# Kernel optimization log

Measured on AMD Instinct MI355X. Metric: run time of the kernel, lower is better.

The kernel has to match this reference:

```python
import jax, jax.numpy as jnp
import numpy as np

B, T, D, H, HD, I = 256, 1, 2048, 16, 128, 5504
EPS = 1e-6
ROPE_THETA = 10000.0


def setup_inputs() -> dict:
    key = jax.random.key(0)
    ks = jax.random.split(key, 20)
    W = 0.02  # weight init scale
    hidden_states = jax.random.normal(ks[0], (B, T, D), jnp.float32)
    # RoPE tables for each batch element at a distinct decode position
    pos = jnp.arange(B, dtype=jnp.float32) % 4096.0
    inv_freq = 1.0 / (ROPE_THETA ** (jnp.arange(0, HD, 2, dtype=jnp.float32) / HD))
    ang = pos[:, None] * inv_freq[None, :]                      # [B, HD/2]
    emb = jnp.concatenate([ang, ang], axis=-1)                  # [B, HD]
    cos = jnp.cos(emb)[:, None, :]                              # [B, 1, HD]
    sin = jnp.sin(emb)[:, None, :]
    n = lambda k, s: jax.random.normal(k, s, jnp.float32) * W
    return {
        'hidden_states': hidden_states, 'cos': cos, 'sin': sin,
        'router_w': n(ks[1], (D,)), 'router_b': jnp.zeros((1,), jnp.float32),
        'ln1_w': jnp.ones((D,), jnp.float32), 'ln2_w': jnp.ones((D,), jnp.float32),
        'wq': n(ks[2], (D, D)), 'bq': jnp.zeros((D,), jnp.float32),
        'wk': n(ks[3], (D, D)), 'bk': jnp.zeros((D,), jnp.float32),
        'wv': n(ks[4], (D, D)), 'bv': jnp.zeros((D,), jnp.float32),
        'wo': n(ks[5], (D, D)),
        'w_gate': n(ks[6], (D, I)), 'w_up': n(ks[7], (D, I)), 'w_down': n(ks[8], (I, D)),
        'k_sel': 128,
    }


def _rms(x, w):
    v = jnp.mean(jnp.square(x), axis=-1, keepdims=True)
    return x * jax.lax.rsqrt(v + EPS) * w


def _rotate_half(x):
    x1, x2 = jnp.split(x, 2, axis=-1)
    return jnp.concatenate([-x2, x1], axis=-1)


def _decoder_layer(x, cs, sn, ln1_w, ln2_w, wq, bq, wk, bk, wv, bv, wo, w_gate, w_up, w_down):
    # x: [k, T, D]; cs/sn: [k, T, HD]
    k = x.shape[0]
    h = _rms(x, ln1_w)
    q = (h @ wq + bq).reshape(k, T, H, HD).transpose(0, 2, 1, 3)  # [k,H,T,HD]
    kk = (h @ wk + bk).reshape(k, T, H, HD).transpose(0, 2, 1, 3)
    v = (h @ wv + bv).reshape(k, T, H, HD).transpose(0, 2, 1, 3)
    c = cs[:, None, :, :]  # [k,1,T,HD]
    s = sn[:, None, :, :]
    q = q * c + _rotate_half(q) * s
    kk = kk * c + _rotate_half(kk) * s
    att = jnp.einsum('bhqd,bhkd->bhqk', q, kk) * (HD ** -0.5)
    p = jax.nn.softmax(att, axis=-1)  # T==1: trivial causal mask
    o = jnp.einsum('bhqk,bhkd->bhqd', p, v).transpose(0, 2, 1, 3).reshape(k, T, D) @ wo
    x = x + o
    h2 = _rms(x, ln2_w)
    mlp = (jax.nn.silu(h2 @ w_gate) * (h2 @ w_up)) @ w_down
    return x + mlp


def reference(hidden_states, cos, sin, router_w, router_b, ln1_w, ln2_w,
              wq, bq, wk, bk, wv, bv, wo, w_gate, w_up, w_down, k_sel):
    # causal router: linear D->1 scores per batch row (T==1 decode step)
    scores = hidden_states[:, 0, :] @ router_w + router_b[0]   # [B]
    probs = jax.nn.sigmoid(scores)
    _, sel_idx = jax.lax.top_k(probs, k_sel)                   # [k]
    x_sel = hidden_states[sel_idx]                             # gather [k,T,D]
    cs, sn = cos[sel_idx], sin[sel_idx]                        # [k,T,HD]
    x_out = _decoder_layer(x_sel, cs, sn, ln1_w, ln2_w, wq, bq, wk, bk,
                           wv, bv, wo, w_gate, w_up, w_down)
    return hidden_states.at[sel_idx].set(x_out)                # scatter back
```

## Files before the change

### kernel.cpp

```cpp
#include <hip/hip_runtime.h>
#include <hip/hip_bf16.h>
#include <stdint.h>


#define D_ 2048
#define I_ 5504
#define NROWS 256
#define KSEL 128

typedef __attribute__((ext_vector_type(8))) short short8;
typedef __attribute__((ext_vector_type(4))) float floatx4;

__device__ __forceinline__ unsigned short f2bf(float f) {
  union { float f; unsigned int u; } v; v.f = f;
  unsigned int r = (v.u + 0x7FFFu + ((v.u >> 16) & 1u)) >> 16;
  return (unsigned short)r;
}

__device__ __forceinline__ unsigned int pk2(float lo, float hi) {
  __hip_bfloat162 h = __float22bfloat162_rn(float2{lo, hi});
  unsigned int u; __builtin_memcpy(&u, &h, 4); return u;
}

__global__ void k_router(const float* __restrict__ hid, const float* __restrict__ rw,
                         const float* __restrict__ rb, float* __restrict__ scores) {
  int b = blockIdx.x, t = threadIdx.x;
  const float* x = hid + (size_t)b * D_;
  float s = 0.f;
  for (int i = t; i < D_; i += 256) s += x[i] * rw[i];
  for (int o = 32; o; o >>= 1) s += __shfl_down(s, o);
  __shared__ float red[4];
  if ((t & 63) == 0) red[t >> 6] = s;
  __syncthreads();
  if (t == 0) scores[b] = red[0] + red[1] + red[2] + red[3] + rb[0];
}

__global__ void k_select(const float* __restrict__ scores, const int* __restrict__ kptr,
                         int* __restrict__ sel, int* __restrict__ pos) {
  __shared__ float sv[NROWS];
  int t = threadIdx.x;
  sv[t] = scores[t];
  __syncthreads();
  float s = sv[t];
  int c = 0;
  for (int j = 0; j < NROWS; ++j) {
    float o = sv[j];
    c += (o > s) || (o == s && j < t);
  }
  int k = *kptr;
  if (c < k) sel[c] = t;
  pos[t] = (c < k) ? c : -1;
}

__global__ void k_rms1(const float* __restrict__ hid, const int* __restrict__ sel,
                       const float* __restrict__ ln1, const float* __restrict__ bv,
                       unsigned short* __restrict__ Hb, float* __restrict__ V,
                       float* __restrict__ X1) {
  int i = blockIdx.x, t = threadIdx.x;
  int r = sel[i];
  const float* x = hid + (size_t)r * D_;
  float xs[8]; float ss = 0.f;
#pragma unroll
  for (int c = 0; c < 8; ++c) { float v = x[t + c * 256]; xs[c] = v; ss += v * v; }
  for (int o = 32; o; o >>= 1) ss += __shfl_down(ss, o);
  __shared__ float red[4];
  if ((t & 63) == 0) red[t >> 6] = ss;
  __syncthreads();
  float inv = rsqrtf((red[0] + red[1] + red[2] + red[3]) * (1.0f / D_) + 1e-6f);
#pragma unroll
  for (int c = 0; c < 8; ++c) {
    int idx = t + c * 256;
    size_t o_ = (size_t)i * D_ + idx;
    Hb[o_] = f2bf(xs[c] * inv * ln1[idx]);
    V[o_] = bv[idx];
    X1[o_] = xs[c];
  }
}

__global__ void k_rms2(const float* __restrict__ X1, const float* __restrict__ ln2,
                       unsigned short* __restrict__ H2b, float* __restrict__ G,
                       float* __restrict__ U) {
  int i = blockIdx.x, t = threadIdx.x;
  const float* x = X1 + (size_t)i * D_;
  float xs[8]; float ss = 0.f;
#pragma unroll
  for (int c = 0; c < 8; ++c) { float v = x[t + c * 256]; xs[c] = v; ss += v * v; }
  for (int o = 32; o; o >>= 1) ss += __shfl_down(ss, o);
  __shared__ float red[4];
  if ((t & 63) == 0) red[t >> 6] = ss;
  __syncthreads();
  float inv = rsqrtf((red[0] + red[1] + red[2] + red[3]) * (1.0f / D_) + 1e-6f);
#pragma unroll
  for (int c = 0; c < 8; ++c) {
    int idx = t + c * 256;
    H2b[(size_t)i * D_ + idx] = f2bf(xs[c] * inv * ln2[idx]);
  }
  for (int j = t; j < I_; j += 256) {
    G[(size_t)i * I_ + j] = 0.f;
    U[(size_t)i * I_ + j] = 0.f;
  }
}

__global__ void k_silu_out(const float* __restrict__ G, const float* __restrict__ U,
                           unsigned short* __restrict__ Mb,
                           const float* __restrict__ X1, const int* __restrict__ pos,
                           const float* __restrict__ hid, float* __restrict__ out) {
  int tid = blockIdx.x * 256 + threadIdx.x;
  int stride = gridDim.x * 256;
  const int nM = KSEL * I_;
  for (int i = tid; i < nM; i += stride) {
    float g = G[i], u = U[i];
    float m = (g / (1.f + expf(-g))) * u;
    Mb[i] = f2bf(m);
  }
  const int nO4 = NROWS * (D_ / 4);
  const float4* X14 = (const float4*)X1;
  const float4* H4 = (const float4*)hid;
  float4* O4 = (float4*)out;
  for (int i = tid; i < nO4; i += stride) {
    int row = i >> 9;
    int c4 = i & 511;
    int p = pos[row];
    O4[i] = (p >= 0) ? X14[(size_t)p * 512 + c4] : H4[i];
  }
}

template<bool AF32, bool DUAL>
__global__ __launch_bounds__(256, 2)
void k_gemm(const void* __restrict__ Ap, const float* __restrict__ B0,
            const float* __restrict__ B1, float* __restrict__ C0,
            float* __restrict__ C1, const int* __restrict__ rowmap,
            int K, int KA, int Kb, int lda, int N, int KT, int ldc) {
  constexpr int ST = 72;
  const int bn = blockIdx.x;
  const int kt0 = blockIdx.y * KT;
  const int kt1 = kt0 + KT;
  const int tid = threadIdx.x;
  const int lane = tid & 63;
  const int wave = tid >> 6;
  const int wm = wave >> 1, wn = wave & 1;
  const int fm = lane & 15, kq = lane >> 4;

  __shared__ alignas(16) unsigned short Asm[128 * ST];
  __shared__ alignas(16) unsigned short Bsm0[32 * ST];
  __shared__ alignas(16) unsigned short Bsm1[DUAL ? 32 * ST : 8];

  floatx4 acc0[4] = {};
  floatx4 acc1[4] = {};

  const int ar = tid >> 1;
  const int ah = (tid & 1) * 32;
  const int bnn = tid & 31;
  const int bk8 = (tid >> 5) * 8;

  const unsigned short* Ab = AF32 ? nullptr : (const unsigned short*)Ap + (size_t)ar * lda + ah;
  const float*          Af = AF32 ? (const float*)Ap + (size_t)ar * lda + ah : nullptr;
  const float* B0c = B0 + (size_t)(bn * 32 + bnn);
  const float* B1c = DUAL ? B1 + (size_t)(bn * 32 + bnn) : nullptr;

  uint4 a4[4];
  float4 af8[8];
  float b0v[8], b1v[8];

  auto load_tile = [&](int kt) {
    if (AF32) {
#pragma unroll
      for (int r = 0; r < 8; ++r) {
        int c0 = kt + ah + r * 4;
        af8[r] = (c0 < KA) ? *(const float4*)(Af + kt + r * 4)
                           : make_float4(0.f, 0.f, 0.f, 0.f);
      }
    } else {
#pragma unroll
      for (int r = 0; r < 4; ++r) {
        int c0 = kt + ah + r * 8;
        a4[r] = (c0 < KA) ? *(const uint4*)(Ab + kt + r * 8)
                          : make_uint4(0u, 0u, 0u, 0u);
      }
    }
#pragma unroll
    for (int j = 0; j < 8; ++j) {
      int kr = kt + bk8 + j; kr = kr < Kb ? kr : Kb - 1;
      b0v[j] = B0c[(size_t)kr * N];
      if (DUAL) b1v[j] = B1c[(size_t)kr * N];
    }
  };

  load_tile(kt0);

  for (int kt = kt0; kt < kt1; kt += 64) {
    __syncthreads();
    {
      uint4* Ad = (uint4*)&Asm[ar * ST + ah];
      if (AF32) {
        uint4 q;
#pragma unroll
        for (int r = 0; r < 4; ++r) {
          q.x = pk2(af8[2 * r].x, af8[2 * r].y);
          q.y = pk2(af8[2 * r].z, af8[2 * r].w);
          q.z = pk2(af8[2 * r + 1].x, af8[2 * r + 1].y);
          q.w = pk2(af8[2 * r + 1].z, af8[2 * r + 1].w);
          Ad[r] = q;
        }
      } else {
#pragma unroll
        for (int r = 0; r < 4; ++r) Ad[r] = a4[r];
      }
      uint4 bq;
      bq.x = pk2(b0v[0], b0v[1]); bq.y = pk2(b0v[2], b0v[3]);
      bq.z = pk2(b0v[4], b0v[5]); bq.w = pk2(b0v[6], b0v[7]);
      *(uint4*)&Bsm0[bnn * ST + bk8] = bq;
      if (DUAL) {
        uint4 cq;
        cq.x = pk2(b1v[0], b1v[1]); cq.y = pk2(b1v[2], b1v[3]);
        cq.z = pk2(b1v[4], b1v[5]); cq.w = pk2(b1v[6], b1v[7]);
        *(uint4*)&Bsm1[bnn * ST + bk8] = cq;
      }
    }
    __syncthreads();
    if (kt + 64 < kt1) load_tile(kt + 64);
    short8 afr[2][4], bf0[2], bf1[2];
#pragma unroll
    for (int s = 0; s < 2; ++s) {
#pragma unroll
      for (int i = 0; i < 4; ++i)
        afr[s][i] = *(const short8*)&Asm[(wm * 64 + i * 16 + fm) * ST + s * 32 + kq * 8];
      bf0[s] = *(const short8*)&Bsm0[(wn * 16 + fm) * ST + s * 32 + kq * 8];
      if (DUAL)
        bf1[s] = *(const short8*)&Bsm1[(wn * 16 + fm) * ST + s * 32 + kq * 8];
    }
#pragma unroll
    for (int s = 0; s < 2; ++s) {
#pragma unroll
      for (int i = 0; i < 4; ++i) {
        acc0[i] = __builtin_amdgcn_mfma_f32_16x16x32_bf16(afr[s][i], bf0[s], acc0[i], 0, 0, 0);
        if (DUAL)
          acc1[i] = __builtin_amdgcn_mfma_f32_16x16x32_bf16(afr[s][i], bf1[s], acc1[i], 0, 0, 0);
      }
    }
  }

#pragma unroll
  for (int i = 0; i < 4; ++i) {
#pragma unroll
    for (int r = 0; r < 4; ++r) {
      int row = wm * 64 + i * 16 + kq * 4 + r;
      size_t rbase = rowmap ? (size_t)rowmap[row] * ldc : (size_t)row * ldc;
      int col = bn * 32 + wn * 16 + fm;
      atomicAdd(&C0[rbase + col], acc0[i][r]);
      if (DUAL) atomicAdd(&C1[rbase + col], acc1[i][r]);
    }
  }
}

extern "C" void kernel_launch(void* const* d_in, const int* in_sizes, int n_in,
                              void* d_out, int out_size, void* d_ws, size_t ws_size,
                              hipStream_t stream) {
  const float* hid = (const float*)d_in[0];
  const float* rw  = (const float*)d_in[3];
  const float* rb  = (const float*)d_in[4];
  const float* ln1 = (const float*)d_in[5];
  const float* ln2 = (const float*)d_in[6];
  const float* wv  = (const float*)d_in[11];
  const float* bv  = (const float*)d_in[12];
  const float* wo  = (const float*)d_in[13];
  const float* wg  = (const float*)d_in[14];
  const float* wu  = (const float*)d_in[15];
  const float* wd  = (const float*)d_in[16];
  const int*   kp  = (const int*)d_in[17];
  float* out = (float*)d_out;

  char* ws = (char*)d_ws;
  float*          scores = (float*)(ws + 0);
  int*            sel    = (int*)(ws + 1024);
  int*            pos    = (int*)(ws + 1536);
  unsigned short* Hb     = (unsigned short*)(ws + 4096);
  float*          V      = (float*)(ws + 528384);
  float*          X1     = (float*)(ws + 1576960);
  unsigned short* H2b    = (unsigned short*)(ws + 2625536);
  float*          G      = (float*)(ws + 3149824);
  float*          U      = (float*)(ws + 5967872);
  unsigned short* Mb     = (unsigned short*)(ws + 8785920);

  k_router<<<256, 256, 0, stream>>>(hid, rw, rb, scores);
  k_select<<<1, 256, 0, stream>>>(scores, kp, sel, pos);
  k_rms1<<<128, 256, 0, stream>>>(hid, sel, ln1, bv, Hb, V, X1);
  k_gemm<false, false><<<dim3(64, 8), 256, 0, stream>>>(
      Hb, wv, nullptr, V, nullptr, nullptr, 2048, 2048, 2048, 2048, 2048, 256, 2048);
  k_gemm<true, false><<<dim3(64, 8), 256, 0, stream>>>(
      V, wo, nullptr, X1, nullptr, nullptr, 2048, 2048, 2048, 2048, 2048, 256, 2048);
  k_rms2<<<128, 256, 0, stream>>>(X1, ln2, H2b, G, U);
  k_gemm<false, true><<<dim3(172, 4), 256, 0, stream>>>(
      H2b, wg, wu, G, U, nullptr, 2048, 2048, 2048, 2048, 5504, 512, 5504);
  k_silu_out<<<1024, 256, 0, stream>>>(G, U, Mb, X1, pos, hid, out);
  k_gemm<false, false><<<dim3(64, 8), 256, 0, stream>>>(
      Mb, wd, nullptr, out, nullptr, sel, 5632, 5504, 5504, 5504, 2048, 704, 2048);
}
```

Before: 294.8 us.

## Replace LDS-tiled split-K GEMM with register double-buffered direct-load MFMA kernel

The GEMM no longer stages tiles in shared memory. Each wave now loads its A fragments and the fp32 B columns straight into registers, double-buffers them across 32-wide K steps, and feeds MFMA on 16-column output tiles. Block IDs are remapped in an XCD-aware way, and shapes become template constants. The change also zeroes G/U in one separate vectorized kernel, vectorizes the router, RMSNorm and SiLU kernels with float4/packed-bf16 stores, and drops the padded K in the down projection. It removes LDS round-trips and barriers, at the cost of redundant B loads across the waves of a block and more atomics per output column.

```diff
diff --git a/kernel.cpp b/kernel.cpp
--- a/kernel.cpp
+++ b/kernel.cpp
@@ -11,23 +11,28 @@
 typedef __attribute__((ext_vector_type(8))) short short8;
 typedef __attribute__((ext_vector_type(4))) float floatx4;
 
-__device__ __forceinline__ unsigned short f2bf(float f) {
-  union { float f; unsigned int u; } v; v.f = f;
-  unsigned int r = (v.u + 0x7FFFu + ((v.u >> 16) & 1u)) >> 16;
-  return (unsigned short)r;
-}
-
 __device__ __forceinline__ unsigned int pk2(float lo, float hi) {
   __hip_bfloat162 h = __float22bfloat162_rn(float2{lo, hi});
   unsigned int u; __builtin_memcpy(&u, &h, 4); return u;
 }
 
+__global__ void k_zero(float4* __restrict__ p, int n4) {
+  int i = blockIdx.x * 256 + threadIdx.x;
+  int st = gridDim.x * 256;
+  for (; i < n4; i += st) p[i] = float4{0.f, 0.f, 0.f, 0.f};
+}
+
 __global__ void k_router(const float* __restrict__ hid, const float* __restrict__ rw,
                          const float* __restrict__ rb, float* __restrict__ scores) {
   int b = blockIdx.x, t = threadIdx.x;
-  const float* x = hid + (size_t)b * D_;
+  const float4* x4 = (const float4*)(hid + (size_t)b * D_);
+  const float4* w4 = (const float4*)rw;
   float s = 0.f;
-  for (int i = t; i < D_; i += 256) s += x[i] * rw[i];
+#pragma unroll
+  for (int c = 0; c < 2; ++c) {
+    float4 xv = x4[t + c * 256], wv = w4[t + c * 256];
+    s += xv.x * wv.x + xv.y * wv.y + xv.z * wv.z + xv.w * wv.w;
+  }
   for (int o = 32; o; o >>= 1) s += __shfl_down(s, o);
   __shared__ float red[4];
   if ((t & 63) == 0) red[t >> 6] = s;
@@ -58,47 +63,50 @@
                        float* __restrict__ X1) {
   int i = blockIdx.x, t = threadIdx.x;
   int r = sel[i];
-  const float* x = hid + (size_t)r * D_;
-  float xs[8]; float ss = 0.f;
-#pragma unroll
-  for (int c = 0; c < 8; ++c) { float v = x[t + c * 256]; xs[c] = v; ss += v * v; }
+  const float4* x4 = (const float4*)(hid + (size_t)r * D_);
+  float4 xa = x4[2 * t], xb = x4[2 * t + 1];
+  float ss = xa.x * xa.x + xa.y * xa.y + xa.z * xa.z + xa.w * xa.w
+           + xb.x * xb.x + xb.y * xb.y + xb.z * xb.z + xb.w * xb.w;
   for (int o = 32; o; o >>= 1) ss += __shfl_down(ss, o);
   __shared__ float red[4];
   if ((t & 63) == 0) red[t >> 6] = ss;
   __syncthreads();
   float inv = rsqrtf((red[0] + red[1] + red[2] + red[3]) * (1.0f / D_) + 1e-6f);
-#pragma unroll
-  for (int c = 0; c < 8; ++c) {
-    int idx = t + c * 256;
-    size_t o_ = (size_t)i * D_ + idx;
-    Hb[o_] = f2bf(xs[c] * inv * ln1[idx]);
-    V[o_] = bv[idx];
-    X1[o_] = xs[c];
-  }
+  const float4* w4 = (const float4*)ln1;
+  float4 wa = w4[2 * t], wb = w4[2 * t + 1];
+  union { unsigned int u[4]; uint4 q; } pk;
+  pk.u[0] = pk2(xa.x * inv * wa.x, xa.y * inv * wa.y);
+  pk.u[1] = pk2(xa.z * inv * wa.z, xa.w * inv * wa.w);
+  pk.u[2] = pk2(xb.x * inv * wb.x, xb.y * inv * wb.y);
+  pk.u[3] = pk2(xb.z * inv * wb.z, xb.w * inv * wb.w);
+  ((uint4*)(Hb + (size_t)i * D_))[t] = pk.q;
+  const float4* b4 = (const float4*)bv;
+  float4* V4 = (float4*)(V + (size_t)i * D_);
+  V4[2 * t] = b4[2 * t]; V4[2 * t + 1] = b4[2 * t + 1];
+  float4* X4 = (float4*)(X1 + (size_t)i * D_);
+  X4[2 * t] = xa; X4[2 * t + 1] = xb;
 }
 
 __global__ void k_rms2(const float* __restrict__ X1, const float* __restrict__ ln2,
-                       unsigned short* __restrict__ H2b, float* __restrict__ G,
-                       float* __restrict__ U) {
+                       unsigned short* __restrict__ H2b) {
   int i = blockIdx.x, t = threadIdx.x;
-  const float* x = X1 + (size_t)i * D_;
-  float xs[8]; float ss = 0.f;
-#pragma unroll
-  for (int c = 0; c < 8; ++c) { float v = x[t + c * 256]; xs[c] = v; ss += v * v; }
+  const float4* x4 = (const float4*)(X1 + (size_t)i * D_);
+  float4 xa = x4[2 * t], xb = x4[2 * t + 1];
+  float ss = xa.x * xa.x + xa.y * xa.y + xa.z * xa.z + xa.w * xa.w
+           + xb.x * xb.x + xb.y * xb.y + xb.z * xb.z + xb.w * xb.w;
   for (int o = 32; o; o >>= 1) ss += __shfl_down(ss, o);
   __shared__ float red[4];
   if ((t & 63) == 0) red[t >> 6] = ss;
   __syncthreads();
   float inv = rsqrtf((red[0] + red[1] + red[2] + red[3]) * (1.0f / D_) + 1e-6f);
-#pragma unroll
-  for (int c = 0; c < 8; ++c) {
-    int idx = t + c * 256;
-    H2b[(size_t)i * D_ + idx] = f2bf(xs[c] * inv * ln2[idx]);
-  }
-  for (int j = t; j < I_; j += 256) {
-    G[(size_t)i * I_ + j] = 0.f;
-    U[(size_t)i * I_ + j] = 0.f;
-  }
+  const float4* w4 = (const float4*)ln2;
+  float4 wa = w4[2 * t], wb = w4[2 * t + 1];
+  union { unsigned int u[4]; uint4 q; } pk;
+  pk.u[0] = pk2(xa.x * inv * wa.x, xa.y * inv * wa.y);
+  pk.u[1] = pk2(xa.z * inv * wa.z, xa.w * inv * wa.w);
+  pk.u[2] = pk2(xb.x * inv * wb.x, xb.y * inv * wb.y);
+  pk.u[3] = pk2(xb.z * inv * wb.z, xb.w * inv * wb.w);
+  ((uint4*)(H2b + (size_t)i * D_))[t] = pk.q;
 }
 
 __global__ void k_silu_out(const float* __restrict__ G, const float* __restrict__ U,
@@ -106,149 +114,142 @@
                            const float* __restrict__ X1, const int* __restrict__ pos,
                            const float* __restrict__ hid, float* __restrict__ out) {
   int tid = blockIdx.x * 256 + threadIdx.x;
-  int stride = gridDim.x * 256;
-  const int nM = KSEL * I_;
-  for (int i = tid; i < nM; i += stride) {
-    float g = G[i], u = U[i];
-    float m = (g / (1.f + expf(-g))) * u;
-    Mb[i] = f2bf(m);
+  const int nM4 = KSEL * I_ / 4;
+  if (tid < nM4) {
+    float4 g = ((const float4*)G)[tid], u = ((const float4*)U)[tid];
+    float m0 = (g.x / (1.f + expf(-g.x))) * u.x;
+    float m1 = (g.y / (1.f + expf(-g.y))) * u.y;
+    float m2 = (g.z / (1.f + expf(-g.z))) * u.z;
+    float m3 = (g.w / (1.f + expf(-g.w))) * u.w;
+    uint2 o; o.x = pk2(m0, m1); o.y = pk2(m2, m3);
+    ((uint2*)Mb)[tid] = o;
   }
   const int nO4 = NROWS * (D_ / 4);
-  const float4* X14 = (const float4*)X1;
-  const float4* H4 = (const float4*)hid;
-  float4* O4 = (float4*)out;
-  for (int i = tid; i < nO4; i += stride) {
-    int row = i >> 9;
-    int c4 = i & 511;
+  if (tid < nO4) {
+    int row = tid >> 9;
+    int c4 = tid & 511;
     int p = pos[row];
-    O4[i] = (p >= 0) ? X14[(size_t)p * 512 + c4] : H4[i];
-  }
-}
-
-template<bool AF32, bool DUAL>
-__global__ __launch_bounds__(256, 2)
+    ((float4*)out)[tid] = (p >= 0) ? ((const float4*)X1)[(size_t)p * 512 + c4]
+                                   : ((const float4*)hid)[tid];
+  }
+}
+
+template<bool AF32, bool DUAL, int SPLITS, int LDA, int NN, int LDC>
+__global__ __launch_bounds__(256, 3)
 void k_gemm(const void* __restrict__ Ap, const float* __restrict__ B0,
             const float* __restrict__ B1, float* __restrict__ C0,
             float* __restrict__ C1, const int* __restrict__ rowmap,
-            int K, int KA, int Kb, int lda, int N, int KT, int ldc) {
-  constexpr int ST = 72;
-  const int bn = blockIdx.x;
-  const int kt0 = blockIdx.y * KT;
-  const int kt1 = kt0 + KT;
-  const int tid = threadIdx.x;
-  const int lane = tid & 63;
-  const int wave = tid >> 6;
-  const int wm = wave >> 1, wn = wave & 1;
-  const int fm = lane & 15, kq = lane >> 4;
-
-  __shared__ alignas(16) unsigned short Asm[128 * ST];
-  __shared__ alignas(16) unsigned short Bsm0[32 * ST];
-  __shared__ alignas(16) unsigned short Bsm1[DUAL ? 32 * ST : 8];
-
-  floatx4 acc0[4] = {};
-  floatx4 acc1[4] = {};
-
-  const int ar = tid >> 1;
-  const int ah = (tid & 1) * 32;
-  const int bnn = tid & 31;
-  const int bk8 = (tid >> 5) * 8;
-
-  const unsigned short* Ab = AF32 ? nullptr : (const unsigned short*)Ap + (size_t)ar * lda + ah;
-  const float*          Af = AF32 ? (const float*)Ap + (size_t)ar * lda + ah : nullptr;
-  const float* B0c = B0 + (size_t)(bn * 32 + bnn);
-  const float* B1c = DUAL ? B1 + (size_t)(bn * 32 + bnn) : nullptr;
-
-  uint4 a4[4];
-  float4 af8[8];
-  float b0v[8], b1v[8];
-
-  auto load_tile = [&](int kt) {
-    if (AF32) {
-#pragma unroll
-      for (int r = 0; r < 8; ++r) {
-        int c0 = kt + ah + r * 4;
-        af8[r] = (c0 < KA) ? *(const float4*)(Af + kt + r * 4)
-                           : make_float4(0.f, 0.f, 0.f, 0.f);
+            int K, int KC) {
+  int nwg = gridDim.x;
+  int id = blockIdx.x;
+  int nid = (id & 7) * (nwg >> 3) + (id >> 3);
+  int bn = nid / SPLITS;
+  int ks = nid % SPLITS;
+  int k0 = ks * KC;
+  int k1 = k0 + KC; if (k1 > K) k1 = K;
+
+  int tid = threadIdx.x;
+  int lane = tid & 63, wq = tid >> 6;
+  int fm = lane & 15, kq = lane >> 4;
+  int colbase = bn * 16;
+
+  const unsigned short* Ab = nullptr;
+  const float* Af = nullptr;
+  if constexpr (AF32) Af = (const float*)Ap + (size_t)(wq * 32 + fm) * LDA + kq * 8;
+  else                Ab = (const unsigned short*)Ap + (size_t)(wq * 32 + fm) * LDA + kq * 8;
+  const float* B0k = B0 + (size_t)(k0 + kq * 8) * NN + colbase + fm;
+  const float* B1k = DUAL ? B1 + (size_t)(k0 + kq * 8) * NN + colbase + fm : nullptr;
+
+  floatx4 acc0[2] = {};
+  floatx4 acc1[2] = {};
+
+  struct Regs {
+    uint4 a[2];
+    float4 af[2][2];
+    float b0[8], b1[8];
+  };
+
+  auto load = [&](Regs& r, int kk) {
+    int dk = kk - k0;
+    if constexpr (AF32) {
+#pragma unroll
+      for (int i = 0; i < 2; ++i) {
+        r.af[i][0] = *(const float4*)(Af + (size_t)(i * 16) * LDA + kk);
+        r.af[i][1] = *(const float4*)(Af + (size_t)(i * 16) * LDA + kk + 4);
       }
     } else {
 #pragma unroll
-      for (int r = 0; r < 4; ++r) {
-        int c0 = kt + ah + r * 8;
-        a4[r] = (c0 < KA) ? *(const uint4*)(Ab + kt + r * 8)
-                          : make_uint4(0u, 0u, 0u, 0u);
-      }
-    }
-#pragma unroll
-    for (int j = 0; j < 8; ++j) {
-      int kr = kt + bk8 + j; kr = kr < Kb ? kr : Kb - 1;
-      b0v[j] = B0c[(size_t)kr * N];
-      if (DUAL) b1v[j] = B1c[(size_t)kr * N];
+      for (int i = 0; i < 2; ++i)
+        r.a[i] = *(const uint4*)(Ab + (size_t)(i * 16) * LDA + kk);
+    }
+    const float* bp = B0k + (size_t)dk * NN;
+#pragma unroll
+    for (int j = 0; j < 8; ++j) r.b0[j] = bp[(size_t)j * NN];
+    if constexpr (DUAL) {
+      const float* cp = B1k + (size_t)dk * NN;
+#pragma unroll
+      for (int j = 0; j < 8; ++j) r.b1[j] = cp[(size_t)j * NN];
     }
   };
 
-  load_tile(kt0);
-
-  for (int kt = kt0; kt < kt1; kt += 64) {
-    __syncthreads();
-    {
-      uint4* Ad = (uint4*)&Asm[ar * ST + ah];
-      if (AF32) {
-        uint4 q;
-#pragma unroll
-        for (int r = 0; r < 4; ++r) {
-          q.x = pk2(af8[2 * r].x, af8[2 * r].y);
-          q.y = pk2(af8[2 * r].z, af8[2 * r].w);
-          q.z = pk2(af8[2 * r + 1].x, af8[2 * r + 1].y);
-          q.w = pk2(af8[2 * r + 1].z, af8[2 * r + 1].w);
-          Ad[r] = q;
-        }
-      } else {
-#pragma unroll
-        for (int r = 0; r < 4; ++r) Ad[r] = a4[r];
-      }
-      uint4 bq;
-      bq.x = pk2(b0v[0], b0v[1]); bq.y = pk2(b0v[2], b0v[3]);
-      bq.z = pk2(b0v[4], b0v[5]); bq.w = pk2(b0v[6], b0v[7]);
-      *(uint4*)&Bsm0[bnn * ST + bk8] = bq;
-      if (DUAL) {
-        uint4 cq;
-        cq.x = pk2(b1v[0], b1v[1]); cq.y = pk2(b1v[2], b1v[3]);
-        cq.z = pk2(b1v[4], b1v[5]); cq.w = pk2(b1v[6], b1v[7]);
-        *(uint4*)&Bsm1[bnn * ST + bk8] = cq;
-      }
-    }
-    __syncthreads();
-    if (kt + 64 < kt1) load_tile(kt + 64);
-    short8 afr[2][4], bf0[2], bf1[2];
-#pragma unroll
-    for (int s = 0; s < 2; ++s) {
-#pragma unroll
-      for (int i = 0; i < 4; ++i)
-        afr[s][i] = *(const short8*)&Asm[(wm * 64 + i * 16 + fm) * ST + s * 32 + kq * 8];
-      bf0[s] = *(const short8*)&Bsm0[(wn * 16 + fm) * ST + s * 32 + kq * 8];
-      if (DUAL)
-        bf1[s] = *(const short8*)&Bsm1[(wn * 16 + fm) * ST + s * 32 + kq * 8];
-    }
-#pragma unroll
-    for (int s = 0; s < 2; ++s) {
-#pragma unroll
-      for (int i = 0; i < 4; ++i) {
-        acc0[i] = __builtin_amdgcn_mfma_f32_16x16x32_bf16(afr[s][i], bf0[s], acc0[i], 0, 0, 0);
-        if (DUAL)
-          acc1[i] = __builtin_amdgcn_mfma_f32_16x16x32_bf16(afr[s][i], bf1[s], acc1[i], 0, 0, 0);
-      }
-    }
-  }
-
-#pragma unroll
-  for (int i = 0; i < 4; ++i) {
+  auto step = [&](Regs& r) {
+    short8 a0, a1, bf0;
+    union { unsigned int u[4]; short8 s; } cv;
+    if constexpr (AF32) {
+      cv.u[0] = pk2(r.af[0][0].x, r.af[0][0].y);
+      cv.u[1] = pk2(r.af[0][0].z, r.af[0][0].w);
+      cv.u[2] = pk2(r.af[0][1].x, r.af[0][1].y);
+      cv.u[3] = pk2(r.af[0][1].z, r.af[0][1].w);
+      a0 = cv.s;
+      cv.u[0] = pk2(r.af[1][0].x, r.af[1][0].y);
+      cv.u[1] = pk2(r.af[1][0].z, r.af[1][0].w);
+      cv.u[2] = pk2(r.af[1][1].x, r.af[1][1].y);
+      cv.u[3] = pk2(r.af[1][1].z, r.af[1][1].w);
+      a1 = cv.s;
+    } else {
+      union { uint4 q; short8 s; } ua;
+      ua.q = r.a[0]; a0 = ua.s;
+      ua.q = r.a[1]; a1 = ua.s;
+    }
+    cv.u[0] = pk2(r.b0[0], r.b0[1]); cv.u[1] = pk2(r.b0[2], r.b0[3]);
+    cv.u[2] = pk2(r.b0[4], r.b0[5]); cv.u[3] = pk2(r.b0[6], r.b0[7]);
+    bf0 = cv.s;
+    acc0[0] = __builtin_amdgcn_mfma_f32_16x16x32_bf16(a0, bf0, acc0[0], 0, 0, 0);
+    acc0[1] = __builtin_amdgcn_mfma_f32_16x16x32_bf16(a1, bf0, acc0[1], 0, 0, 0);
+    if constexpr (DUAL) {
+      short8 bf1;
+      cv.u[0] = pk2(r.b1[0], r.b1[1]); cv.u[1] = pk2(r.b1[2], r.b1[3]);
+      cv.u[2] = pk2(r.b1[4], r.b1[5]); cv.u[3] = pk2(r.b1[6], r.b1[7]);
+      bf1 = cv.s;
+      acc1[0] = __builtin_amdgcn_mfma_f32_16x16x32_bf16(a0, bf1, acc1[0], 0, 0, 0);
+      acc1[1] = __builtin_amdgcn_mfma_f32_16x16x32_bf16(a1, bf1, acc1[1], 0, 0, 0);
+    }
+  };
+
+  Regs ra, rb;
+  load(ra, k0);
+  int kk = k0;
+  while (true) {
+    int nk = kk + 32;
+    if (nk < k1) load(rb, nk);
+    step(ra);
+    if (nk >= k1) break;
+    kk = nk; nk += 32;
+    if (nk < k1) load(ra, nk);
+    step(rb);
+    if (nk >= k1) break;
+    kk = nk;
+  }
+
+#pragma unroll
+  for (int i = 0; i < 2; ++i) {
 #pragma unroll
     for (int r = 0; r < 4; ++r) {
-      int row = wm * 64 + i * 16 + kq * 4 + r;
-      size_t rbase = rowmap ? (size_t)rowmap[row] * ldc : (size_t)row * ldc;
-      int col = bn * 32 + wn * 16 + fm;
+      int row = wq * 32 + i * 16 + kq * 4 + r;
+      size_t rbase = rowmap ? (size_t)rowmap[row] * LDC : (size_t)row * LDC;
+      int col = colbase + fm;
       atomicAdd(&C0[rbase + col], acc0[i][r]);
-      if (DUAL) atomicAdd(&C1[rbase + col], acc1[i][r]);
+      if constexpr (DUAL) atomicAdd(&C1[rbase + col], acc1[i][r]);
     }
   }
 }
@@ -282,17 +283,18 @@
   float*          U      = (float*)(ws + 5967872);
   unsigned short* Mb     = (unsigned short*)(ws + 8785920);
 
+  k_zero<<<1024, 256, 0, stream>>>((float4*)G, 352256);
   k_router<<<256, 256, 0, stream>>>(hid, rw, rb, scores);
   k_select<<<1, 256, 0, stream>>>(scores, kp, sel, pos);
   k_rms1<<<128, 256, 0, stream>>>(hid, sel, ln1, bv, Hb, V, X1);
-  k_gemm<false, false><<<dim3(64, 8), 256, 0, stream>>>(
-      Hb, wv, nullptr, V, nullptr, nullptr, 2048, 2048, 2048, 2048, 2048, 256, 2048);
-  k_gemm<true, false><<<dim3(64, 8), 256, 0, stream>>>(
-      V, wo, nullptr, X1, nullptr, nullptr, 2048, 2048, 2048, 2048, 2048, 256, 2048);
-  k_rms2<<<128, 256, 0, stream>>>(X1, ln2, H2b, G, U);
-  k_gemm<false, true><<<dim3(172, 4), 256, 0, stream>>>(
-      H2b, wg, wu, G, U, nullptr, 2048, 2048, 2048, 2048, 5504, 512, 5504);
+  k_gemm<false, false, 8, 2048, 2048, 2048><<<1024, 256, 0, stream>>>(
+      Hb, wv, nullptr, V, nullptr, nullptr, 2048, 256);
+  k_gemm<true, false, 8, 2048, 2048, 2048><<<1024, 256, 0, stream>>>(
+      V, wo, nullptr, X1, nullptr, nullptr, 2048, 256);
+  k_rms2<<<128, 256, 0, stream>>>(X1, ln2, H2b);
+  k_gemm<false, true, 4, 2048, 5504, 5504><<<1376, 256, 0, stream>>>(
+      H2b, wg, wu, G, U, nullptr, 2048, 512);
   k_silu_out<<<1024, 256, 0, stream>>>(G, U, Mb, X1, pos, hid, out);
-  k_gemm<false, false><<<dim3(64, 8), 256, 0, stream>>>(
-      Mb, wd, nullptr, out, nullptr, sel, 5632, 5504, 5504, 5504, 2048, 704, 2048);
-}
+  k_gemm<false, false, 8, 5504, 2048, 2048><<<1024, 256, 0, stream>>>(
+      Mb, wd, nullptr, out, nullptr, sel, 5504, 704);
+}
```

New measurement: 357.7 us. +21.3%, slower.

## Double split-K, coalesce GEMM A-tile loads, and vectorize elementwise kernels

Applied to the files above, without the earlier changes.

Doubles the split-K factor of every GEMM launch and raises the launch-bounds occupancy hint from 2 to 4 blocks. The A-tile loaders are remapped so neighbouring threads read consecutive columns of a row, making those global loads coalesced. The router, RMSNorm and SiLU kernels are rewritten to use float4 loads and packed bf16 stores. Zeroing of the G/U accumulators moves out of rms2 into a separate grid-wide kernel. The cost is more atomic partial-sum traffic and possible register-pressure spills under the tighter occupancy hint.

```diff
diff --git a/kernel.cpp b/kernel.cpp
--- a/kernel.cpp
+++ b/kernel.cpp
@@ -11,23 +11,28 @@
 typedef __attribute__((ext_vector_type(8))) short short8;
 typedef __attribute__((ext_vector_type(4))) float floatx4;
 
-__device__ __forceinline__ unsigned short f2bf(float f) {
-  union { float f; unsigned int u; } v; v.f = f;
-  unsigned int r = (v.u + 0x7FFFu + ((v.u >> 16) & 1u)) >> 16;
-  return (unsigned short)r;
-}
-
 __device__ __forceinline__ unsigned int pk2(float lo, float hi) {
   __hip_bfloat162 h = __float22bfloat162_rn(float2{lo, hi});
   unsigned int u; __builtin_memcpy(&u, &h, 4); return u;
 }
 
+__global__ void k_zero(float4* __restrict__ p, int n4) {
+  int i = blockIdx.x * 256 + threadIdx.x;
+  int st = gridDim.x * 256;
+  for (; i < n4; i += st) p[i] = float4{0.f, 0.f, 0.f, 0.f};
+}
+
 __global__ void k_router(const float* __restrict__ hid, const float* __restrict__ rw,
                          const float* __restrict__ rb, float* __restrict__ scores) {
   int b = blockIdx.x, t = threadIdx.x;
-  const float* x = hid + (size_t)b * D_;
+  const float4* x4 = (const float4*)(hid + (size_t)b * D_);
+  const float4* w4 = (const float4*)rw;
   float s = 0.f;
-  for (int i = t; i < D_; i += 256) s += x[i] * rw[i];
+#pragma unroll
+  for (int c = 0; c < 2; ++c) {
+    float4 xv = x4[t + c * 256], wv = w4[t + c * 256];
+    s += xv.x * wv.x + xv.y * wv.y + xv.z * wv.z + xv.w * wv.w;
+  }
   for (int o = 32; o; o >>= 1) s += __shfl_down(s, o);
   __shared__ float red[4];
   if ((t & 63) == 0) red[t >> 6] = s;
@@ -58,47 +63,50 @@
                        float* __restrict__ X1) {
   int i = blockIdx.x, t = threadIdx.x;
   int r = sel[i];
-  const float* x = hid + (size_t)r * D_;
-  float xs[8]; float ss = 0.f;
-#pragma unroll
-  for (int c = 0; c < 8; ++c) { float v = x[t + c * 256]; xs[c] = v; ss += v * v; }
+  const float4* x4 = (const float4*)(hid + (size_t)r * D_);
+  float4 xa = x4[2 * t], xb = x4[2 * t + 1];
+  float ss = xa.x * xa.x + xa.y * xa.y + xa.z * xa.z + xa.w * xa.w
+           + xb.x * xb.x + xb.y * xb.y + xb.z * xb.z + xb.w * xb.w;
   for (int o = 32; o; o >>= 1) ss += __shfl_down(ss, o);
   __shared__ float red[4];
   if ((t & 63) == 0) red[t >> 6] = ss;
   __syncthreads();
   float inv = rsqrtf((red[0] + red[1] + red[2] + red[3]) * (1.0f / D_) + 1e-6f);
-#pragma unroll
-  for (int c = 0; c < 8; ++c) {
-    int idx = t + c * 256;
-    size_t o_ = (size_t)i * D_ + idx;
-    Hb[o_] = f2bf(xs[c] * inv * ln1[idx]);
-    V[o_] = bv[idx];
-    X1[o_] = xs[c];
-  }
+  const float4* w4 = (const float4*)ln1;
+  float4 wa = w4[2 * t], wb = w4[2 * t + 1];
+  union { unsigned int u[4]; uint4 q; } pk;
+  pk.u[0] = pk2(xa.x * inv * wa.x, xa.y * inv * wa.y);
+  pk.u[1] = pk2(xa.z * inv * wa.z, xa.w * inv * wa.w);
+  pk.u[2] = pk2(xb.x * inv * wb.x, xb.y * inv * wb.y);
+  pk.u[3] = pk2(xb.z * inv * wb.z, xb.w * inv * wb.w);
+  ((uint4*)(Hb + (size_t)i * D_))[t] = pk.q;
+  const float4* b4 = (const float4*)bv;
+  float4* V4 = (float4*)(V + (size_t)i * D_);
+  V4[2 * t] = b4[2 * t]; V4[2 * t + 1] = b4[2 * t + 1];
+  float4* X4 = (float4*)(X1 + (size_t)i * D_);
+  X4[2 * t] = xa; X4[2 * t + 1] = xb;
 }
 
 __global__ void k_rms2(const float* __restrict__ X1, const float* __restrict__ ln2,
-                       unsigned short* __restrict__ H2b, float* __restrict__ G,
-                       float* __restrict__ U) {
+                       unsigned short* __restrict__ H2b) {
   int i = blockIdx.x, t = threadIdx.x;
-  const float* x = X1 + (size_t)i * D_;
-  float xs[8]; float ss = 0.f;
-#pragma unroll
-  for (int c = 0; c < 8; ++c) { float v = x[t + c * 256]; xs[c] = v; ss += v * v; }
+  const float4* x4 = (const float4*)(X1 + (size_t)i * D_);
+  float4 xa = x4[2 * t], xb = x4[2 * t + 1];
+  float ss = xa.x * xa.x + xa.y * xa.y + xa.z * xa.z + xa.w * xa.w
+           + xb.x * xb.x + xb.y * xb.y + xb.z * xb.z + xb.w * xb.w;
   for (int o = 32; o; o >>= 1) ss += __shfl_down(ss, o);
   __shared__ float red[4];
   if ((t & 63) == 0) red[t >> 6] = ss;
   __syncthreads();
   float inv = rsqrtf((red[0] + red[1] + red[2] + red[3]) * (1.0f / D_) + 1e-6f);
-#pragma unroll
-  for (int c = 0; c < 8; ++c) {
-    int idx = t + c * 256;
-    H2b[(size_t)i * D_ + idx] = f2bf(xs[c] * inv * ln2[idx]);
-  }
-  for (int j = t; j < I_; j += 256) {
-    G[(size_t)i * I_ + j] = 0.f;
-    U[(size_t)i * I_ + j] = 0.f;
-  }
+  const float4* w4 = (const float4*)ln2;
+  float4 wa = w4[2 * t], wb = w4[2 * t + 1];
+  union { unsigned int u[4]; uint4 q; } pk;
+  pk.u[0] = pk2(xa.x * inv * wa.x, xa.y * inv * wa.y);
+  pk.u[1] = pk2(xa.z * inv * wa.z, xa.w * inv * wa.w);
+  pk.u[2] = pk2(xb.x * inv * wb.x, xb.y * inv * wb.y);
+  pk.u[3] = pk2(xb.z * inv * wb.z, xb.w * inv * wb.w);
+  ((uint4*)(H2b + (size_t)i * D_))[t] = pk.q;
 }
 
 __global__ void k_silu_out(const float* __restrict__ G, const float* __restrict__ U,
@@ -106,27 +114,28 @@
                            const float* __restrict__ X1, const int* __restrict__ pos,
                            const float* __restrict__ hid, float* __restrict__ out) {
   int tid = blockIdx.x * 256 + threadIdx.x;
-  int stride = gridDim.x * 256;
-  const int nM = KSEL * I_;
-  for (int i = tid; i < nM; i += stride) {
-    float g = G[i], u = U[i];
-    float m = (g / (1.f + expf(-g))) * u;
-    Mb[i] = f2bf(m);
+  const int nM4 = KSEL * I_ / 4;
+  if (tid < nM4) {
+    float4 g = ((const float4*)G)[tid], u = ((const float4*)U)[tid];
+    float m0 = (g.x / (1.f + expf(-g.x))) * u.x;
+    float m1 = (g.y / (1.f + expf(-g.y))) * u.y;
+    float m2 = (g.z / (1.f + expf(-g.z))) * u.z;
+    float m3 = (g.w / (1.f + expf(-g.w))) * u.w;
+    uint2 o; o.x = pk2(m0, m1); o.y = pk2(m2, m3);
+    ((uint2*)Mb)[tid] = o;
   }
   const int nO4 = NROWS * (D_ / 4);
-  const float4* X14 = (const float4*)X1;
-  const float4* H4 = (const float4*)hid;
-  float4* O4 = (float4*)out;
-  for (int i = tid; i < nO4; i += stride) {
-    int row = i >> 9;
-    int c4 = i & 511;
+  if (tid < nO4) {
+    int row = tid >> 9;
+    int c4 = tid & 511;
     int p = pos[row];
-    O4[i] = (p >= 0) ? X14[(size_t)p * 512 + c4] : H4[i];
+    ((float4*)out)[tid] = (p >= 0) ? ((const float4*)X1)[(size_t)p * 512 + c4]
+                                   : ((const float4*)hid)[tid];
   }
 }
 
 template<bool AF32, bool DUAL>
-__global__ __launch_bounds__(256, 2)
+__global__ __launch_bounds__(256, 4)
 void k_gemm(const void* __restrict__ Ap, const float* __restrict__ B0,
             const float* __restrict__ B1, float* __restrict__ C0,
             float* __restrict__ C1, const int* __restrict__ rowmap,
@@ -148,13 +157,15 @@
   floatx4 acc0[4] = {};
   floatx4 acc1[4] = {};
 
-  const int ar = tid >> 1;
-  const int ah = (tid & 1) * 32;
+  const int arow = tid >> 3;
+  const int akg  = (tid & 7) * 8;
+  const int frow = tid >> 4;
+  const int fkg  = (tid & 15) * 4;
   const int bnn = tid & 31;
   const int bk8 = (tid >> 5) * 8;
 
-  const unsigned short* Ab = AF32 ? nullptr : (const unsigned short*)Ap + (size_t)ar * lda + ah;
-  const float*          Af = AF32 ? (const float*)Ap + (size_t)ar * lda + ah : nullptr;
+  const unsigned short* Ab = AF32 ? nullptr : (const unsigned short*)Ap;
+  const float*          Af = AF32 ? (const float*)Ap : nullptr;
   const float* B0c = B0 + (size_t)(bn * 32 + bnn);
   const float* B1c = DUAL ? B1 + (size_t)(bn * 32 + bnn) : nullptr;
 
@@ -164,18 +175,20 @@
 
   auto load_tile = [&](int kt) {
     if (AF32) {
+      const int c0 = kt + fkg;
+      const bool ok = c0 < KA;
 #pragma unroll
       for (int r = 0; r < 8; ++r) {
-        int c0 = kt + ah + r * 4;
-        af8[r] = (c0 < KA) ? *(const float4*)(Af + kt + r * 4)
-                           : make_float4(0.f, 0.f, 0.f, 0.f);
+        const float* p = Af + (size_t)(r * 16 + frow) * lda + c0;
+        af8[r] = ok ? *(const float4*)p : make_float4(0.f, 0.f, 0.f, 0.f);
       }
     } else {
+      const int c0 = kt + akg;
+      const bool ok = c0 < KA;
 #pragma unroll
       for (int r = 0; r < 4; ++r) {
-        int c0 = kt + ah + r * 8;
-        a4[r] = (c0 < KA) ? *(const uint4*)(Ab + kt + r * 8)
-                          : make_uint4(0u, 0u, 0u, 0u);
+        const unsigned short* p = Ab + (size_t)(r * 32 + arow) * lda + c0;
+        a4[r] = ok ? *(const uint4*)p : make_uint4(0u, 0u, 0u, 0u);
       }
     }
 #pragma unroll
@@ -191,20 +204,18 @@
   for (int kt = kt0; kt < kt1; kt += 64) {
     __syncthreads();
     {
-      uint4* Ad = (uint4*)&Asm[ar * ST + ah];
       if (AF32) {
-        uint4 q;
-#pragma unroll
-        for (int r = 0; r < 4; ++r) {
-          q.x = pk2(af8[2 * r].x, af8[2 * r].y);
-          q.y = pk2(af8[2 * r].z, af8[2 * r].w);
-          q.z = pk2(af8[2 * r + 1].x, af8[2 * r + 1].y);
-          q.w = pk2(af8[2 * r + 1].z, af8[2 * r + 1].w);
-          Ad[r] = q;
+#pragma unroll
+        for (int r = 0; r < 8; ++r) {
+          uint2 w;
+          w.x = pk2(af8[r].x, af8[r].y);
+          w.y = pk2(af8[r].z, af8[r].w);
+          *(uint2*)&Asm[(r * 16 + frow) * ST + fkg] = w;
         }
       } else {
 #pragma unroll
-        for (int r = 0; r < 4; ++r) Ad[r] = a4[r];
+        for (int r = 0; r < 4; ++r)
+          *(uint4*)&Asm[(r * 32 + arow) * ST + akg] = a4[r];
       }
       uint4 bq;
       bq.x = pk2(b0v[0], b0v[1]); bq.y = pk2(b0v[2], b0v[3]);
@@ -282,17 +293,18 @@
   float*          U      = (float*)(ws + 5967872);
   unsigned short* Mb     = (unsigned short*)(ws + 8785920);
 
+  k_zero<<<1024, 256, 0, stream>>>((float4*)G, 352256);
   k_router<<<256, 256, 0, stream>>>(hid, rw, rb, scores);
   k_select<<<1, 256, 0, stream>>>(scores, kp, sel, pos);
   k_rms1<<<128, 256, 0, stream>>>(hid, sel, ln1, bv, Hb, V, X1);
-  k_gemm<false, false><<<dim3(64, 8), 256, 0, stream>>>(
-      Hb, wv, nullptr, V, nullptr, nullptr, 2048, 2048, 2048, 2048, 2048, 256, 2048);
-  k_gemm<true, false><<<dim3(64, 8), 256, 0, stream>>>(
-      V, wo, nullptr, X1, nullptr, nullptr, 2048, 2048, 2048, 2048, 2048, 256, 2048);
-  k_rms2<<<128, 256, 0, stream>>>(X1, ln2, H2b, G, U);
-  k_gemm<false, true><<<dim3(172, 4), 256, 0, stream>>>(
-      H2b, wg, wu, G, U, nullptr, 2048, 2048, 2048, 2048, 5504, 512, 5504);
+  k_gemm<false, false><<<dim3(64, 16), 256, 0, stream>>>(
+      Hb, wv, nullptr, V, nullptr, nullptr, 2048, 2048, 2048, 2048, 2048, 128, 2048);
+  k_gemm<true, false><<<dim3(64, 16), 256, 0, stream>>>(
+      V, wo, nullptr, X1, nullptr, nullptr, 2048, 2048, 2048, 2048, 2048, 128, 2048);
+  k_rms2<<<128, 256, 0, stream>>>(X1, ln2, H2b);
+  k_gemm<false, true><<<dim3(172, 8), 256, 0, stream>>>(
+      H2b, wg, wu, G, U, nullptr, 2048, 2048, 2048, 2048, 5504, 256, 5504);
   k_silu_out<<<1024, 256, 0, stream>>>(G, U, Mb, X1, pos, hid, out);
-  k_gemm<false, false><<<dim3(64, 8), 256, 0, stream>>>(
-      Mb, wd, nullptr, out, nullptr, sel, 5632, 5504, 5504, 5504, 2048, 704, 2048);
-}
+  k_gemm<false, false><<<dim3(64, 16), 256, 0, stream>>>(
+      Mb, wd, nullptr, out, nullptr, sel, 6144, 5504, 5504, 5504, 2048, 384, 2048);
+}
```

New measurement: 309.1 us. 4.9% more time.
